# Optimization experiments

Hardware: AMD Instinct MI355X
Metric: run time of the kernel (lower is better)

The kernel has to match this reference:

```python
import jax, jax.numpy as jnp
import numpy as np

H = 1024      # hidden_dim
V = 50257     # vocab_size
E = 512       # embedding_dim
PAD = 0       # padding_idx
B = 128       # batch
S = 512       # src_len


def setup_inputs() -> dict:
    key = jax.random.key(0)
    ks = jax.random.split(key, 16)
    sc = 0.02
    emb_table = jax.random.normal(ks[0], (V, E), jnp.float32) * sc
    emb_table = emb_table.at[PAD].set(0.0)  # padding_idx row is zero
    return {
        "decoder_input": jax.random.randint(ks[1], (B,), 0, V),
        "decoder_hidden": jax.random.normal(ks[2], (1, B, H), jnp.float32),
        "encoder_outputs": jax.random.normal(ks[3], (B, S, 2 * H), jnp.float32),
        "emb_table": emb_table,
        "W_ah": jax.random.normal(ks[4], (H, H), jnp.float32) * sc,
        "b_ah": jnp.zeros((H,), jnp.float32),
        "W_ae": jax.random.normal(ks[5], (H, 2 * H), jnp.float32) * sc,
        "b_ae": jnp.zeros((H,), jnp.float32),
        "w_score": jax.random.normal(ks[6], (H,), jnp.float32) * sc,
        "W_ih": jax.random.normal(ks[7], (3 * H, E + 2 * H), jnp.float32) * sc,
        "W_hh": jax.random.normal(ks[8], (3 * H, H), jnp.float32) * sc,
        "b_ih": jnp.zeros((3 * H,), jnp.float32),
        "b_hh": jnp.zeros((3 * H,), jnp.float32),
        "W_out": jax.random.normal(ks[9], (V, H), jnp.float32) * sc,
        "b_out": jnp.zeros((V,), jnp.float32),
    }


def reference(decoder_input, decoder_hidden, encoder_outputs, emb_table,
              W_ah, b_ah, W_ae, b_ae, w_score, W_ih, W_hh, b_ih, b_hh,
              W_out, b_out):
    h = decoder_hidden[0]                                  # [B,H]
    emb = emb_table[decoder_input]                         # [B,E]

    # Bahdanau attention
    ah = h @ W_ah.T + b_ah                                 # [B,H]
    ae = jnp.einsum('bsd,hd->bsh', encoder_outputs, W_ae) + b_ae  # [B,S,H]
    scores = jnp.tanh(ah[:, None, :] + ae) @ w_score       # [B,S]
    attn = jax.nn.softmax(scores, axis=1)                  # [B,S]
    ctx = jnp.einsum('bs,bsd->bd', attn, encoder_outputs)  # [B,2H]

    # GRU single step (PyTorch gate layout: r, z, n)
    x = jnp.concatenate([emb, ctx], axis=1)                # [B,E+2H]
    gx = x @ W_ih.T + b_ih                                 # [B,3H]
    gh = h @ W_hh.T + b_hh                                 # [B,3H]
    r = jax.nn.sigmoid(gx[:, :H] + gh[:, :H])
    z = jax.nn.sigmoid(gx[:, H:2 * H] + gh[:, H:2 * H])
    n = jnp.tanh(gx[:, 2 * H:] + r * gh[:, 2 * H:])
    h_new = (1.0 - z) * n + z * h                          # [B,H]

    out = h_new @ W_out.T + b_out                          # [B,V]
    return out[:, None, :], h_new[None]                    # [B,1,V], [1,B,H]
```

## Files before the change

kernel.cpp:

```cpp
#include <hip/hip_runtime.h>
#include <hip/hip_bf16.h>

#define DEVI __device__ __forceinline__

typedef short bf16x8 __attribute__((ext_vector_type(8)));
typedef float f32x4  __attribute__((ext_vector_type(4)));

static constexpr int Bb   = 128;
static constexpr int Ss   = 512;
static constexpr int Hh   = 1024;
static constexpr int Ee   = 512;
static constexpr int Vv   = 50257;
static constexpr int TWOH = 2048;

DEVI short f2bf(float f){ __hip_bfloat16 h = __float2bfloat16(f); return *reinterpret_cast<short*>(&h); }
DEVI float bf2f(short s){ __hip_bfloat16 h = *reinterpret_cast<__hip_bfloat16*>(&s); return __bfloat162float(h); }

DEVI float tanh_fast(float x){
  float e = __expf(2.0f*x);
  return 1.0f - 2.0f/(e + 1.0f);
}

DEVI bf16x8 pack8(f32x4 a, f32x4 b){
  bf16x8 v;
  v[0]=f2bf(a[0]); v[1]=f2bf(a[1]); v[2]=f2bf(a[2]); v[3]=f2bf(a[3]);
  v[4]=f2bf(b[0]); v[5]=f2bf(b[1]); v[6]=f2bf(b[2]); v[7]=f2bf(b[3]);
  return v;
}

DEVI void gld_lds16(const void* g, void* l){
  __builtin_amdgcn_global_load_lds((const __attribute__((address_space(1))) void*)g,
                                   (__attribute__((address_space(3))) void*)l, 16, 0, 0);
}

DEVI f32x4 mfma16(bf16x8 a, bf16x8 b, f32x4 c){
  return __builtin_amdgcn_mfma_f32_16x16x32_bf16(a, b, c, 0, 0, 0);
}

__global__ void k_enc2bf(const float* __restrict__ enc, short* __restrict__ encb)
{
  const size_t i = ((size_t)blockIdx.x*256 + threadIdx.x) * 8;
  f32x4 f0 = *(const f32x4*)(enc + i);
  f32x4 f1 = *(const f32x4*)(enc + i + 4);
  *(bf16x8*)(encb + i) = pack8(f0, f1);
}

__global__ void k_prep(const float* __restrict__ wae, short* __restrict__ waeb,
                       const float* __restrict__ h, short* __restrict__ hb,
                       const int* __restrict__ dec_in, const float* __restrict__ emb,
                       short* __restrict__ xb)
{
  const int total_wae = Hh*TWOH;
  const int total_h   = Bb*Hh;
  const int total_emb = Bb*Ee;
  const int total = total_wae + total_h + total_emb;
  for (int i = blockIdx.x*blockDim.x + threadIdx.x; i < total; i += gridDim.x*blockDim.x){
    if (i < total_wae) waeb[i] = f2bf(wae[i]);
    else if (i < total_wae + total_h){ int j = i - total_wae; hb[j] = f2bf(h[j]); }
    else {
      int j = i - total_wae - total_h;
      int b = j >> 9, e = j & 511;
      xb[b*2560 + e] = f2bf(emb[(size_t)dec_in[b]*Ee + e]);
    }
  }
}

__launch_bounds__(512)
__global__ void k_scores8(const short* __restrict__ encbf, const short* __restrict__ waeb,
                          const float* __restrict__ ahb, const float* __restrict__ b_ah,
                          const float* __restrict__ b_ae, const float* __restrict__ wsc,
                          float* __restrict__ scores)
{
  __shared__ __align__(16) char LDSB[163840];
  const int q  = blockIdx.x;
  const int xcd = q & 7, sl = q >> 3;
  const int rt = xcd*32 + (sl>>2), nb = sl & 3;
  const int tid = threadIdx.x, wid = tid>>6, lane = tid&63;
  const int wr = wid>>2, wc = wid&3;
  const int srow = lane>>3, l7 = lane&7;
  const int lo = lane&15, hi4 = lane>>4;
  const int swk = (l7 ^ srow)*8;

  const short* Ag = encbf + (size_t)rt*256*TWOH + (size_t)(wid*8+srow)*TWOH + swk;
  const short* Bg = waeb  + (size_t)nb*256*TWOH + (size_t)(wid*8+srow)*TWOH + swk;
  char* AW = LDSB + wid*1024;
  char* BW = LDSB + 98304 + wid*1024;
  const char* AR = LDSB + (wr*128 + lo)*128;
  const char* BR = LDSB + 98304 + (wc*64 + lo)*128;
  const int sw0 = (hi4*16) ^ (l7<<4);
  const int sw1 = (64 + hi4*16) ^ (l7<<4);

  f32x4 acc[8][4] = {};

  auto STA = [&](int buf, int kt, int hp){
    #pragma unroll
    for (int i=0;i<2;++i){
      int rnd = hp*2+i;
      gld_lds16(Ag + (size_t)rnd*64*TWOH + kt*64, AW + buf*32768 + rnd*8192);
    }
  };
  auto STB = [&](int buf, int kt, int hp){
    #pragma unroll
    for (int i=0;i<2;++i){
      int rnd = hp*2+i;
      gld_lds16(Bg + (size_t)rnd*64*TWOH + kt*64, BW + buf*32768 + rnd*8192);
    }
  };

  STA(0,0,0); STA(0,0,1);
  STB(0,0,0); STB(0,0,1);
  STA(1,1,0); STA(1,1,1);
  asm volatile("s_waitcnt vmcnt(4)" ::: "memory");
  __builtin_amdgcn_s_barrier();
  __builtin_amdgcn_sched_barrier(0);

  int ab = 0;
  for (int t = 0; t < 32; ++t){
    int ab2 = ab+2; if (ab2>=3) ab2-=3;
    const int aO = ab*32768, bO = (t&1)*32768;
    bf16x8 af[4], bq[4];

    if (t<31){ STB((t+1)&1, t+1, 0); STB((t+1)&1, t+1, 1); }
    #pragma unroll
    for (int j=0;j<4;++j) bq[j] = *(const bf16x8*)(BR + bO + j*2048 + sw0);
    #pragma unroll
    for (int i=0;i<4;++i) af[i] = *(const bf16x8*)(AR + aO + i*2048 + sw0);
    __builtin_amdgcn_s_setprio(1);
    #pragma unroll
    for (int i=0;i<4;++i)
      #pragma unroll
      for (int j=0;j<4;++j)
        acc[i][j] = mfma16(af[i], bq[j], acc[i][j]);
    __builtin_amdgcn_s_setprio(0);
    #pragma unroll
    for (int i=0;i<4;++i) af[i] = *(const bf16x8*)(AR + aO + (4+i)*2048 + sw0);
    __builtin_amdgcn_s_setprio(1);
    #pragma unroll
    for (int i=0;i<4;++i)
      #pragma unroll
      for (int j=0;j<4;++j)
        acc[4+i][j] = mfma16(af[i], bq[j], acc[4+i][j]);
    __builtin_amdgcn_s_setprio(0);
    __builtin_amdgcn_s_barrier();

    if (t<30){ STA(ab2, t+2, 0); STA(ab2, t+2, 1); }
    #pragma unroll
    for (int j=0;j<4;++j) bq[j] = *(const bf16x8*)(BR + bO + j*2048 + sw1);
    #pragma unroll
    for (int i=0;i<4;++i) af[i] = *(const bf16x8*)(AR + aO + i*2048 + sw1);
    __builtin_amdgcn_s_setprio(1);
    #pragma unroll
    for (int i=0;i<4;++i)
      #pragma unroll
      for (int j=0;j<4;++j)
        acc[i][j] = mfma16(af[i], bq[j], acc[i][j]);
    __builtin_amdgcn_s_setprio(0);
    #pragma unroll
    for (int i=0;i<4;++i) af[i] = *(const bf16x8*)(AR + aO + (4+i)*2048 + sw1);
    __builtin_amdgcn_s_setprio(1);
    #pragma unroll
    for (int i=0;i<4;++i)
      #pragma unroll
      for (int j=0;j<4;++j)
        acc[4+i][j] = mfma16(af[i], bq[j], acc[4+i][j]);
    __builtin_amdgcn_s_setprio(0);
    if (t<30)       asm volatile("s_waitcnt vmcnt(4)" ::: "memory");
    else if (t==30) asm volatile("s_waitcnt vmcnt(0)" ::: "memory");
    __builtin_amdgcn_s_barrier();
    __builtin_amdgcn_sched_barrier(0);

    ab = (ab==2) ? 0 : ab+1;
  }
  const int b = rt >> 1;
  float w4[4], t4[4];
  #pragma unroll
  for (int j=0;j<4;++j){
    int n = nb*256 + wc*64 + j*16 + lo;
    w4[j] = wsc[n];
    t4[j] = ahb[b*Hh + n] + b_ah[n] + b_ae[n];
  }
  #pragma unroll
  for (int i=0;i<8;++i){
    #pragma unroll
    for (int q2=0;q2<4;++q2){
      int m = rt*256 + wr*128 + i*16 + hi4*4 + q2;
      float s = 0.f;
      #pragma unroll
      for (int j=0;j<4;++j) s += tanh_fast(t4[j] + acc[i][j][q2]) * w4[j];
      s += __shfl_xor(s,1); s += __shfl_xor(s,2); s += __shfl_xor(s,4); s += __shfl_xor(s,8);
      if (lo == 0) atomicAdd(&scores[m], s);
    }
  }
}

__launch_bounds__(512)
__global__ void k_scores_f32(const float* __restrict__ enc, const short* __restrict__ waeb,
                             const float* __restrict__ ahb, const float* __restrict__ b_ah,
                             const float* __restrict__ b_ae, const float* __restrict__ wsc,
                             float* __restrict__ scores)
{
  __shared__ __align__(16) short As[2][128*64];
  __shared__ __align__(16) short Bs[2][256*64];
  const int p  = blockIdx.x;
  const int rt = p >> 2, nb = p & 3;
  const int tid = threadIdx.x, wid = tid>>6, lane = tid&63;
  const int wr = wid>>2, wc = wid&3;
  const int srow = lane>>3, l7 = lane&7;
  const int swk = (l7 ^ srow) * 8;
  f32x4 acc[4][4] = {};
  const float* Af  = enc  + (size_t)rt*128*TWOH;
  const short* Bbp = waeb + (size_t)nb*256*TWOH;
  f32x4 pa0[2], pa1[2];

  auto stageB = [&](int s, int kt){
    #pragma unroll
    for (int i=0;i<4;++i){
      int c = wid*4+i, row = c*8+srow;
      gld_lds16(Bbp + (size_t)row*TWOH + kt*64 + swk, (char*)Bs[s] + c*1024);
    }
  };
  auto prefA = [&](int kt){
    #pragma unroll
    for (int i=0;i<2;++i){
      int row = (wid*2+i)*8+srow;
      const float* bp = Af + (size_t)row*TWOH + kt*64 + l7*8;
      pa0[i] = *(const f32x4*)bp; pa1[i] = *(const f32x4*)(bp+4);
    }
  };
  auto commitA = [&](int s){
    #pragma unroll
    for (int i=0;i<2;++i){
      int row = (wid*2+i)*8+srow;
      *(bf16x8*)((char*)As[s] + row*128 + ((l7^srow)<<4)) = pack8(pa0[i], pa1[i]);
    }
  };

  prefA(0); commitA(0); stageB(0,0);
  __syncthreads();
  int cur = 0;
  for (int kt=0; kt<32; ++kt){
    if (kt<31){ prefA(kt+1); stageB(cur^1, kt+1); }
    #pragma unroll
    for (int kk=0;kk<2;++kk){
      bf16x8 af[4], bq[4];
      const int sw = (kk*64 + (lane>>4)*16) ^ (l7<<4);
      #pragma unroll
      for (int i=0;i<4;++i) af[i] = *(const bf16x8*)((const char*)As[cur] + (wr*64+i*16+(lane&15))*128 + sw);
      #pragma unroll
      for (int j=0;j<4;++j) bq[j] = *(const bf16x8*)((const char*)Bs[cur] + (wc*64+j*16+(lane&15))*128 + sw);
      #pragma unroll
      for (int i=0;i<4;++i)
        #pragma unroll
        for (int j=0;j<4;++j)
          acc[i][j] = mfma16(af[i], bq[j], acc[i][j]);
    }
    if (kt<31) commitA(cur^1);
    __syncthreads();
    cur ^= 1;
  }
  const int lo = lane&15, hi = lane>>4;
  const int b = rt>>2;
  float w4[4], t4[4];
  #pragma unroll
  for (int j=0;j<4;++j){
    int n = nb*256 + wc*64 + j*16 + lo;
    w4[j] = wsc[n];
    t4[j] = ahb[b*Hh + n] + b_ah[n] + b_ae[n];
  }
  #pragma unroll
  for (int i=0;i<4;++i){
    #pragma unroll
    for (int q2=0;q2<4;++q2){
      int m = rt*128 + wr*64 + i*16 + hi*4 + q2;
      float s = 0.f;
      #pragma unroll
      for (int j=0;j<4;++j) s += tanhf(t4[j] + acc[i][j][q2]) * w4[j];
      s += __shfl_xor(s,1); s += __shfl_xor(s,2); s += __shfl_xor(s,4); s += __shfl_xor(s,8);
      if (lo == 0) atomicAdd(&scores[m], s);
    }
  }
}

template<int MODE>
__launch_bounds__(256)
__global__ void k_gemm128(const short* __restrict__ A, int lda,
                          const float* __restrict__ B0, const float* __restrict__ B1,
                          float* __restrict__ O0, float* __restrict__ O1,
                          const float* __restrict__ bias, int kiters)
{
  __shared__ __align__(16) short As[2][128*64];
  __shared__ __align__(16) short Bs[2][128*64];
  const int nb = blockIdx.x;
  const int tid = threadIdx.x, wid = tid>>6, lane = tid&63;
  const int wr = wid>>1, wc = wid&1;
  const int srow = lane>>3, l7 = lane&7;
  const int swk = (l7 ^ srow) * 8;

  const float* Bt; int noff; float* Ot; int ostride;
  if constexpr (MODE==0){
    if (nb < 8){ Bt = B0; noff = 0;    Ot = O0; ostride = Hh;   }
    else       { Bt = B1; noff = 1024; Ot = O1; ostride = 3*Hh; }
  } else if constexpr (MODE==1){ Bt = B0; noff = 0; Ot = O0; ostride = 3*Hh; }
  else { Bt = B0; noff = 0; Ot = O0; ostride = Vv; }

  f32x4 acc[4][4] = {};
  f32x4 pb0[4], pb1[4];

  auto stageA = [&](int s, int kt){
    #pragma unroll
    for (int i=0;i<4;++i){
      int c = wid*4+i, row = c*8+srow;
      gld_lds16(A + (size_t)row*lda + kt*64 + swk, (char*)As[s] + c*1024);
    }
  };
  auto prefB = [&](int kt){
    #pragma unroll
    for (int i=0;i<4;++i){
      int row = (wid*4+i)*8+srow;
      int n = nb*128 + row - noff;
      if constexpr (MODE==2) n = (n > Vv-1) ? (Vv-1) : n;
      const float* bp = Bt + (size_t)n*lda + kt*64 + l7*8;
      pb0[i] = *(const f32x4*)bp; pb1[i] = *(const f32x4*)(bp+4);
    }
  };
  auto commitB = [&](int s){
    #pragma unroll
    for (int i=0;i<4;++i){
      int row = (wid*4+i)*8+srow;
      *(bf16x8*)((char*)Bs[s] + row*128 + ((l7^srow)<<4)) = pack8(pb0[i], pb1[i]);
    }
  };

  const int kt0 = blockIdx.y * kiters, kend = kt0 + kiters;
  stageA(0, kt0); prefB(kt0); commitB(0);
  __syncthreads();

  int cur = 0;
  for (int kt = kt0; kt < kend; ++kt){
    if (kt+1 < kend){ stageA(cur^1, kt+1); prefB(kt+1); }
    #pragma unroll
    for (int kk=0;kk<2;++kk){
      bf16x8 af[4], bq[4];
      const int sw = (kk*64 + (lane>>4)*16) ^ (l7<<4);
      #pragma unroll
      for (int i=0;i<4;++i) af[i] = *(const bf16x8*)((const char*)As[cur] + (wr*64+i*16+(lane&15))*128 + sw);
      #pragma unroll
      for (int j=0;j<4;++j) bq[j] = *(const bf16x8*)((const char*)Bs[cur] + (wc*64+j*16+(lane&15))*128 + sw);
      #pragma unroll
      for (int i=0;i<4;++i)
        #pragma unroll
        for (int j=0;j<4;++j)
          acc[i][j] = mfma16(af[i], bq[j], acc[i][j]);
    }
    if (kt+1 < kend) commitB(cur^1);
    __syncthreads();
    cur ^= 1;
  }
  const int lo = lane&15, hi = lane>>4;
  #pragma unroll
  for (int i=0;i<4;++i){
    #pragma unroll
    for (int j=0;j<4;++j){
      int n = nb*128 + wc*64 + j*16 + lo - noff;
      #pragma unroll
      for (int q=0;q<4;++q){
        int m = wr*64 + i*16 + hi*4 + q;
        float v = acc[i][j][q];
        if constexpr (MODE==2){
          if (n < Vv) O0[(size_t)m*Vv + n] = v + bias[n];
        } else {
          atomicAdd(&Ot[(size_t)m*ostride + n], v);
        }
      }
    }
  }
}

__global__ void k_softmax(const float* __restrict__ scores, float* __restrict__ attn)
{
  __shared__ float red[512];
  const int b = blockIdx.x, tid = threadIdx.x;
  float v = scores[b*Ss + tid];
  red[tid] = v; __syncthreads();
  for (int off=256; off>0; off>>=1){ if (tid<off) red[tid] = fmaxf(red[tid], red[tid+off]); __syncthreads(); }
  float mx = red[0]; __syncthreads();
  float e = __expf(v - mx);
  red[tid] = e; __syncthreads();
  for (int off=256; off>0; off>>=1){ if (tid<off) red[tid] += red[tid+off]; __syncthreads(); }
  attn[b*Ss + tid] = e / red[0];
}

__global__ void k_ctx_bf16(const short* __restrict__ encb, const float* __restrict__ attn,
                           float* __restrict__ ctxp)
{
  __shared__ float a[128];
  const int bid = blockIdx.x, b = bid>>2, ch = bid&3, tid = threadIdx.x;
  if (tid < 128) a[tid] = attn[b*Ss + ch*128 + tid];
  __syncthreads();
  const short* e0 = encb + (size_t)(b*Ss + ch*128)*TWOH + tid*8;
  float s[8] = {};
  for (int r=0; r<128; ++r){
    bf16x8 v = *(const bf16x8*)(e0 + (size_t)r*TWOH);
    float w = a[r];
    #pragma unroll
    for (int j=0;j<8;++j) s[j] += w * bf2f(v[j]);
  }
  float* o = ctxp + (size_t)ch*Bb*TWOH + (size_t)b*TWOH + tid*8;
  #pragma unroll
  for (int j=0;j<8;++j) o[j] = s[j];
}

__global__ void k_ctxfin(const float* __restrict__ ctxp, short* __restrict__ xb)
{
  const int g = blockIdx.x*256 + threadIdx.x;
  const int b = g >> 11, col = g & 2047;
  const int N = Bb*TWOH;
  float v = ctxp[g] + ctxp[N+g] + ctxp[2*N+g] + ctxp[3*N+g];
  xb[b*2560 + 512 + col] = f2bf(v);
}

__global__ void k_ctx_f32(const float* __restrict__ enc, const float* __restrict__ attn,
                          short* __restrict__ xb)
{
  __shared__ float a[512];
  const int ch = blockIdx.x, b = blockIdx.y, tid = threadIdx.x;
  a[tid]     = attn[b*Ss + tid];
  a[tid+256] = attn[b*Ss + tid + 256];
  __syncthreads();
  const float* e0 = enc + (size_t)b*Ss*TWOH + ch*256 + tid;
  float s0=0.f, s1=0.f, s2=0.f, s3=0.f;
  for (int s=0; s<512; s+=4){
    s0 += a[s]   * e0[(size_t)(s  )*TWOH];
    s1 += a[s+1] * e0[(size_t)(s+1)*TWOH];
    s2 += a[s+2] * e0[(size_t)(s+2)*TWOH];
    s3 += a[s+3] * e0[(size_t)(s+3)*TWOH];
  }
  xb[b*2560 + 512 + ch*256 + tid] = f2bf(s0+s1+s2+s3);
}

__global__ void k_gates(const float* __restrict__ gx, const float* __restrict__ gh,
                        const float* __restrict__ b_ih, const float* __restrict__ b_hh,
                        const float* __restrict__ h, float* __restrict__ hnew_out,
                        short* __restrict__ hnewb)
{
  const int gid = blockIdx.x*256 + threadIdx.x;
  const int b = gid >> 10, j = gid & 1023;
  float xr = gx[b*3072 + j]        + b_ih[j];
  float xz = gx[b*3072 + 1024 + j] + b_ih[1024+j];
  float xn = gx[b*3072 + 2048 + j] + b_ih[2048+j];
  float hr = gh[b*3072 + j]        + b_hh[j];
  float hz = gh[b*3072 + 1024 + j] + b_hh[1024+j];
  float hn = gh[b*3072 + 2048 + j] + b_hh[2048+j];
  float r = 1.f/(1.f + __expf(-(xr+hr)));
  float z = 1.f/(1.f + __expf(-(xz+hz)));
  float n = tanhf(xn + r*hn);
  float hv = (1.f - z)*n + z*h[b*Hh + j];
  hnew_out[gid] = hv;
  hnewb[gid] = f2bf(hv);
}

extern "C" void kernel_launch(void* const* d_in, const int* in_sizes, int n_in,
                              void* d_out, int out_size, void* d_ws, size_t ws_size,
                              hipStream_t stream)
{
  const int*   dec   = (const int*)  d_in[0];
  const float* h     = (const float*)d_in[1];
  const float* enc   = (const float*)d_in[2];
  const float* emb   = (const float*)d_in[3];
  const float* W_ah  = (const float*)d_in[4];
  const float* b_ah  = (const float*)d_in[5];
  const float* W_ae  = (const float*)d_in[6];
  const float* b_ae  = (const float*)d_in[7];
  const float* wsc   = (const float*)d_in[8];
  const float* W_ih  = (const float*)d_in[9];
  const float* W_hh  = (const float*)d_in[10];
  const float* b_ih  = (const float*)d_in[11];
  const float* b_hh  = (const float*)d_in[12];
  const float* W_out = (const float*)d_in[13];
  const float* b_out = (const float*)d_in[14];
  float* out = (float*)d_out;
  float* hnew_out = out + (size_t)Bb*Vv;

  char* w = (char*)d_ws;
  float* scores = (float*)w;  w += (size_t)65536*4;
  float* ahb    = (float*)w;  w += (size_t)131072*4;
  float* ghb    = (float*)w;  w += (size_t)393216*4;
  float* gxb    = (float*)w;  w += (size_t)393216*4;
  size_t zero_bytes = (size_t)(w - (char*)d_ws);
  float* attn   = (float*)w;  w += (size_t)65536*4;
  short* waeb   = (short*)w;  w += (size_t)2097152*2;
  short* xb     = (short*)w;  w += (size_t)128*2560*2;
  short* hb     = (short*)w;  w += (size_t)131072*2;
  short* hnb    = (short*)w;  w += (size_t)131072*2;
  float* ctxp   = (float*)w;  w += (size_t)4*Bb*TWOH*4;
  short* encb   = (short*)w;  w += (size_t)65536*2048*2;
  const bool big = ((size_t)(w - (char*)d_ws) <= ws_size);

  hipMemsetAsync(d_ws, 0, zero_bytes, stream);
  if (big) k_enc2bf<<<65536, 256, 0, stream>>>(enc, encb);
  k_prep<<<4096, 256, 0, stream>>>(W_ae, waeb, h, hb, dec, emb, xb);
  k_gemm128<0><<<dim3(32,2), 256, 0, stream>>>(hb, 1024, W_ah, W_hh, ahb, ghb, nullptr, 8);
  if (big)
    k_scores8<<<1024, 512, 0, stream>>>(encb, waeb, ahb, b_ah, b_ae, wsc, scores);
  else
    k_scores_f32<<<2048, 512, 0, stream>>>(enc, waeb, ahb, b_ah, b_ae, wsc, scores);
  k_softmax<<<128, 512, 0, stream>>>(scores, attn);
  if (big){
    k_ctx_bf16<<<512, 256, 0, stream>>>(encb, attn, ctxp);
    k_ctxfin<<<1024, 256, 0, stream>>>(ctxp, xb);
  } else {
    k_ctx_f32<<<dim3(8,128), 256, 0, stream>>>(enc, attn, xb);
  }
  k_gemm128<1><<<dim3(24,4), 256, 0, stream>>>(xb, 2560, W_ih, nullptr, gxb, nullptr, nullptr, 10);
  k_gates<<<512, 256, 0, stream>>>(gxb, ghb, b_ih, b_hh, h, hnew_out, hnb);
  k_gemm128<2><<<dim3(393,1), 256, 0, stream>>>(hnb, 1024, W_out, nullptr, out, nullptr, b_out, 16);
}
```

Measured before the change: 547.8 us.

## Load W_ae operand directly from global into registers in scores GEMM

The attention-score GEMM no longer stages the W_ae (B) tiles through LDS. Each wave now reads its B fragments straight from global memory into registers every k-step, and all A prefetches are issued in one batch after the compute. This shrinks LDS use from 160KB to 96KB and removes one barrier per iteration. The cost is duplicated global/L2 reads of B across waves. Because the memory counter drains in issue order, waiting on the direct B loads may also force waiting on in-flight A prefetches, exposing memory latency.

```diff
diff --git a/kernel.cpp b/kernel.cpp
--- a/kernel.cpp
+++ b/kernel.cpp
@@ -71,7 +71,7 @@
                           const float* __restrict__ b_ae, const float* __restrict__ wsc,
                           float* __restrict__ scores)
 {
-  __shared__ __align__(16) char LDSB[163840];
+  __shared__ __align__(16) char LDSB[98304];
   const int q  = blockIdx.x;
   const int xcd = q & 7, sl = q >> 3;
   const int rt = xcd*32 + (sl>>2), nb = sl & 3;
@@ -81,35 +81,22 @@
   const int lo = lane&15, hi4 = lane>>4;
   const int swk = (l7 ^ srow)*8;
 
-  const short* Ag = encbf + (size_t)rt*256*TWOH + (size_t)(wid*8+srow)*TWOH + swk;
-  const short* Bg = waeb  + (size_t)nb*256*TWOH + (size_t)(wid*8+srow)*TWOH + swk;
+  const short* Ag  = encbf + (size_t)rt*256*TWOH + (size_t)(wid*8+srow)*TWOH + swk;
+  const short* Bgr = waeb  + (size_t)nb*256*TWOH + (size_t)(wc*64+lo)*TWOH + hi4*8;
   char* AW = LDSB + wid*1024;
-  char* BW = LDSB + 98304 + wid*1024;
   const char* AR = LDSB + (wr*128 + lo)*128;
-  const char* BR = LDSB + 98304 + (wc*64 + lo)*128;
   const int sw0 = (hi4*16) ^ (l7<<4);
   const int sw1 = (64 + hi4*16) ^ (l7<<4);
 
   f32x4 acc[8][4] = {};
 
-  auto STA = [&](int buf, int kt, int hp){
-    #pragma unroll
-    for (int i=0;i<2;++i){
-      int rnd = hp*2+i;
+  auto STA = [&](int buf, int kt){
+    #pragma unroll
+    for (int rnd=0; rnd<4; ++rnd)
       gld_lds16(Ag + (size_t)rnd*64*TWOH + kt*64, AW + buf*32768 + rnd*8192);
-    }
-  };
-  auto STB = [&](int buf, int kt, int hp){
-    #pragma unroll
-    for (int i=0;i<2;++i){
-      int rnd = hp*2+i;
-      gld_lds16(Bg + (size_t)rnd*64*TWOH + kt*64, BW + buf*32768 + rnd*8192);
-    }
-  };
-
-  STA(0,0,0); STA(0,0,1);
-  STB(0,0,0); STB(0,0,1);
-  STA(1,1,0); STA(1,1,1);
+  };
+
+  STA(0,0); STA(1,1);
   asm volatile("s_waitcnt vmcnt(4)" ::: "memory");
   __builtin_amdgcn_s_barrier();
   __builtin_amdgcn_sched_barrier(0);
@@ -117,12 +104,12 @@
   int ab = 0;
   for (int t = 0; t < 32; ++t){
     int ab2 = ab+2; if (ab2>=3) ab2-=3;
-    const int aO = ab*32768, bO = (t&1)*32768;
+    const int aO = ab*32768;
+    const short* Bk = Bgr + t*64;
     bf16x8 af[4], bq[4];
 
-    if (t<31){ STB((t+1)&1, t+1, 0); STB((t+1)&1, t+1, 1); }
-    #pragma unroll
-    for (int j=0;j<4;++j) bq[j] = *(const bf16x8*)(BR + bO + j*2048 + sw0);
+    #pragma unroll
+    for (int j=0;j<4;++j) bq[j] = *(const bf16x8*)(Bk + (size_t)j*16*TWOH);
     #pragma unroll
     for (int i=0;i<4;++i) af[i] = *(const bf16x8*)(AR + aO + i*2048 + sw0);
     __builtin_amdgcn_s_setprio(1);
@@ -141,11 +128,9 @@
       for (int j=0;j<4;++j)
         acc[4+i][j] = mfma16(af[i], bq[j], acc[4+i][j]);
     __builtin_amdgcn_s_setprio(0);
-    __builtin_amdgcn_s_barrier();
-
-    if (t<30){ STA(ab2, t+2, 0); STA(ab2, t+2, 1); }
-    #pragma unroll
-    for (int j=0;j<4;++j) bq[j] = *(const bf16x8*)(BR + bO + j*2048 + sw1);
+
+    #pragma unroll
+    for (int j=0;j<4;++j) bq[j] = *(const bf16x8*)(Bk + (size_t)j*16*TWOH + 32);
     #pragma unroll
     for (int i=0;i<4;++i) af[i] = *(const bf16x8*)(AR + aO + i*2048 + sw1);
     __builtin_amdgcn_s_setprio(1);
@@ -164,6 +149,8 @@
       for (int j=0;j<4;++j)
         acc[4+i][j] = mfma16(af[i], bq[j], acc[4+i][j]);
     __builtin_amdgcn_s_setprio(0);
+
+    if (t<30) STA(ab2, t+2);
     if (t<30)       asm volatile("s_waitcnt vmcnt(4)" ::: "memory");
     else if (t==30) asm volatile("s_waitcnt vmcnt(0)" ::: "memory");
     __builtin_amdgcn_s_barrier();
```

After: 668.3 us. +22.0%, slower.
